# Kernel tuning notes

Measured on AMD Instinct MI355X. Metric: run time of the kernel, lower is better.

The kernel has to match this reference:

```python
import jax, jax.numpy as jnp
import numpy as np

BLANK = 1   # Offsets.GO
NEG = -1e30  # effective -inf that stays finite under logaddexp


def setup_inputs() -> dict:
    key = jax.random.key(0)
    k1, k2, k3, k4 = jax.random.split(key, 4)
    T, B, V, S = 1000, 64, 512, 100
    logits = jax.random.normal(k1, (T, B, V), dtype=jnp.float32)
    log_prob = jax.nn.log_softmax(logits, axis=-1)  # ctc_loss expects log-probs
    input_lengths = jax.random.randint(k2, (B,), T // 2, T + 1, dtype=jnp.int32)
    # target tokens avoid PAD(0)/GO(1,blank)/EOS(2), matching the masked_select semantics
    targets = jax.random.randint(k3, (B, S), 3, V, dtype=jnp.int32)
    target_lengths = jax.random.randint(k4, (B,), S // 2, S + 1, dtype=jnp.int32)
    return {"log_prob": log_prob, "input_lengths": input_lengths,
            "targets": targets, "target_lengths": target_lengths}


def _ctc_loss_sum(log_prob, input_lengths, targets, target_lengths):
    # log_prob: (T, B, V) log-softmax outputs; targets: (B, S) padded labels
    T, B, V = log_prob.shape
    S = targets.shape[1]
    Se = 2 * S + 1  # extended label sequence: blank-interleaved

    ext = jnp.full((B, Se), BLANK, dtype=targets.dtype).at[:, 1::2].set(targets)
    pos = jnp.arange(Se)
    ext_len = 2 * target_lengths + 1                      # (B,)
    valid = pos[None, :] < ext_len[:, None]               # (B, Se)
    ext_m2 = jnp.pad(ext[:, :-2], ((0, 0), (2, 0)), constant_values=BLANK)
    allow_skip = (ext != BLANK) & (ext != ext_m2) & (pos[None, :] >= 2)

    # emit[t, b, s] = log_prob[t, b, ext[b, s]]  -> (T, B, Se)
    emit = jnp.take_along_axis(log_prob, jnp.broadcast_to(ext[None], (T, B, Se)), axis=2)

    # alpha init at t=0
    alpha = jnp.full((B, Se), NEG, dtype=log_prob.dtype)
    alpha = alpha.at[:, 0].set(emit[0, :, 0])
    alpha = alpha.at[:, 1].set(jnp.where(target_lengths > 0, emit[0, :, 1], NEG))
    alpha = jnp.where(valid, alpha, NEG)

    def step(alpha, xt):
        emit_t, t = xt
        a1 = alpha
        a2 = jnp.pad(alpha[:, :-1], ((0, 0), (1, 0)), constant_values=NEG)
        a3 = jnp.where(allow_skip,
                       jnp.pad(alpha[:, :-2], ((0, 0), (2, 0)), constant_values=NEG),
                       NEG)
        new = jnp.logaddexp(jnp.logaddexp(a1, a2), a3) + emit_t
        new = jnp.where(valid, new, NEG)
        # freeze alpha once past each sample's input length
        alpha = jnp.where((t < input_lengths)[:, None], new, alpha)
        return alpha, None

    alpha, _ = jax.lax.scan(step, alpha, (emit[1:], jnp.arange(1, T)))

    last = 2 * target_lengths  # index of trailing blank in extended sequence
    a_last = jnp.take_along_axis(alpha, last[:, None], axis=1)[:, 0]
    a_prev = jnp.take_along_axis(alpha, jnp.maximum(last - 1, 0)[:, None], axis=1)[:, 0]
    loglik = jnp.logaddexp(a_last, a_prev)
    loss = -loglik
    # zero_infinity=True: infeasible alignments contribute 0
    loss = jnp.where(loglik < 0.5 * NEG, 0.0, loss)
    return jnp.sum(loss)  # reduction='sum'


def reference(log_prob, input_lengths, targets, target_lengths):
    return _ctc_loss_sum(log_prob, input_lengths, targets, target_lengths)
```

## Files before the change

### kernel.cpp

```cpp
#include <hip/hip_runtime.h>


#define NEGF (-1e30f)

constexpr int CT_T  = 1000;
constexpr int CT_B  = 64;
constexpr int CT_V  = 512;
constexpr int CT_S  = 100;
constexpr int CT_Se = 201;
constexpr float LOG2E = 1.4426950408889634f;
constexpr float LN2   = 0.6931471805599453f;
constexpr float SHIFT = 5.0f;

#if __has_builtin(__builtin_amdgcn_exp2f) && __has_builtin(__builtin_amdgcn_logf)
__device__ __forceinline__ float fexp2(float x) { return __builtin_amdgcn_exp2f(x); }
__device__ __forceinline__ float flog2(float x) { return __builtin_amdgcn_logf(x); }
__device__ __forceinline__ float frcp(float x)  { return __builtin_amdgcn_rcpf(x); }
#else
__device__ __forceinline__ float fexp2(float x) { return exp2f(x); }
__device__ __forceinline__ float flog2(float x) { return log2f(x); }
__device__ __forceinline__ float frcp(float x)  { return 1.0f / x; }
#endif

__device__ __forceinline__ float lae2_b2(float x, float y) {
    float m = fmaxf(x, y);
    float d = fminf(x, y) - m;
    return m + flog2(1.0f + fexp2(d));
}
__device__ __forceinline__ float lae3_b2(float x, float y, float z) {
    float m = fmaxf(fmaxf(x, y), z);
    float s = fexp2(x - m) + fexp2(y - m) + fexp2(z - m);
    return m + flog2(s);
}

__device__ __forceinline__ float wave_shr1(float x) {
    return __int_as_float(__builtin_amdgcn_update_dpp(
        0, __float_as_int(x), 0x138, 0xf, 0xf, true));
}
__device__ __forceinline__ float wave_max_nonneg(float x) {
#define DPPMAX(ctrl) x = fmaxf(x, __int_as_float(__builtin_amdgcn_update_dpp( \
        0, __float_as_int(x), ctrl, 0xf, 0xf, true)))
    DPPMAX(0x111); DPPMAX(0x112); DPPMAX(0x114); DPPMAX(0x118);
    DPPMAX(0x142); DPPMAX(0x143);
#undef DPPMAX
    return __int_as_float(__builtin_amdgcn_readlane(__float_as_int(x), 63));
}

typedef const __attribute__((address_space(1))) unsigned int* as1_uint_ptr;
typedef __attribute__((address_space(3))) unsigned int* as3_uint_ptr;
__device__ __forceinline__ void gld16(const void* g, void* l) {
    __builtin_amdgcn_global_load_lds((as1_uint_ptr)g, (as3_uint_ptr)l, 16, 0, 0);
}
__device__ __forceinline__ void waitcnt_vm32() { __builtin_amdgcn_s_waitcnt(0x8F70); }
__device__ __forceinline__ void waitcnt_vm0()  { __builtin_amdgcn_s_waitcnt(0x0F70); }

__global__ __launch_bounds__(64, 1) void ctc_alpha(
    const float* __restrict__ logp,
    const int*   __restrict__ in_len,
    const int*   __restrict__ tgt,
    const int*   __restrict__ tgt_len,
    float*       __restrict__ loss_ws)
{
    __shared__ float ldsr[4][8][CT_V];

    const int b    = blockIdx.x;
    const int lane = threadIdx.x;
    const int Tin  = in_len[b];
    const int Lt   = tgt_len[b];
    const int lim  = 2 * Lt + 1;
    const int* tg  = tgt + b * CT_S;

    const int s0 = 4 * lane, s1 = s0 + 1, s3 = s0 + 3;
    const int i1 = min((s1 - 1) >> 1, CT_S - 1);
    const int i3 = min((s3 - 1) >> 1, CT_S - 1);
    const int c1 = tg[i1];
    const int c3 = tg[i3];
    const float sk1 = ((s1 >= 3) && (s1 < CT_Se) && (c1 != tg[max(i1 - 1, 0)])) ? 1.f : 0.f;
    const float sk3 = ((s3 >= 3) && (s3 < CT_Se) && (c3 != tg[max(i3 - 1, 0)])) ? 1.f : 0.f;
    const float m0 = (s0     < lim) ? 1.f : 0.f;
    const float m1 = (s0 + 1 < lim) ? 1.f : 0.f;
    const float m2 = (s0 + 2 < lim) ? 1.f : 0.f;
    const float m3 = (s0 + 3 < lim) ? 1.f : 0.f;

    float a0 = 0.f, a1 = 0.f, a2 = 0.f, a3 = 0.f, pa3 = 0.f;
    if (lane == 0) {
        const float* r0 = logp + (size_t)b * CT_V;
        a0 = fexp2(fmaf(r0[1], LOG2E, SHIFT));
        if (Lt > 0) a1 = fexp2(fmaf(r0[c1], LOG2E, SHIFT));
    }
    float rs = 0.f;

    auto issue = [&](int k, int buf) {
        const int tb = 1 + 8 * k;
        #pragma unroll
        for (int i = 0; i < 8; ++i) {
            const int t = min(tb + i, CT_T - 1);
            const char* g = (const char*)(logp + ((size_t)t * CT_B + b) * CT_V)
                          + (size_t)lane * 16;
            gld16(g,        &ldsr[buf][i][0]);
            gld16(g + 1024, &ldsr[buf][i][256]);
        }
    };

    auto renorm = [&]() {
        float lm = wave_max_nonneg(fmaxf(fmaxf(a0, a1), fmaxf(a2, a3)));
        if (lm > 0.f) {
            float sc = frcp(lm);
            rs += flog2(lm);
            a0 *= sc; a1 *= sc; a2 *= sc; a3 *= sc;
            pa3 = wave_shr1(a3);
        }
    };

    auto run8 = [&](int buf, int tb, bool guard) {
        unsigned base = (unsigned)(size_t)(&ldsr[buf][0][0]);
        unsigned ab = base + 4u * 1;
        unsigned a1a = base + 4u * (unsigned)c1;
        unsigned a3a = base + 4u * (unsigned)c3;
        float g0,g1,g2,g3,g4,g5,g6,g7,g8,g9,g10,g11,
              g12,g13,g14,g15,g16,g17,g18,g19,g20,g21,g22,g23;
        asm volatile(
            "ds_read_b32 %0,  %24 offset:0\n\t"
            "ds_read_b32 %1,  %25 offset:0\n\t"
            "ds_read_b32 %2,  %26 offset:0\n\t"
            "ds_read_b32 %3,  %24 offset:2048\n\t"
            "ds_read_b32 %4,  %25 offset:2048\n\t"
            "ds_read_b32 %5,  %26 offset:2048\n\t"
            "ds_read_b32 %6,  %24 offset:4096\n\t"
            "ds_read_b32 %7,  %25 offset:4096\n\t"
            "ds_read_b32 %8,  %26 offset:4096\n\t"
            "ds_read_b32 %9,  %24 offset:6144\n\t"
            "ds_read_b32 %10, %25 offset:6144\n\t"
            "ds_read_b32 %11, %26 offset:6144\n\t"
            "ds_read_b32 %12, %24 offset:8192\n\t"
            "ds_read_b32 %13, %25 offset:8192\n\t"
            "ds_read_b32 %14, %26 offset:8192\n\t"
            "ds_read_b32 %15, %24 offset:10240\n\t"
            "ds_read_b32 %16, %25 offset:10240\n\t"
            "ds_read_b32 %17, %26 offset:10240\n\t"
            "ds_read_b32 %18, %24 offset:12288\n\t"
            "ds_read_b32 %19, %25 offset:12288\n\t"
            "ds_read_b32 %20, %26 offset:12288\n\t"
            "ds_read_b32 %21, %24 offset:14336\n\t"
            "ds_read_b32 %22, %25 offset:14336\n\t"
            "ds_read_b32 %23, %26 offset:14336\n\t"
            "s_waitcnt lgkmcnt(0)"
            : "=&v"(g0), "=&v"(g1), "=&v"(g2), "=&v"(g3), "=&v"(g4), "=&v"(g5),
              "=&v"(g6), "=&v"(g7), "=&v"(g8), "=&v"(g9), "=&v"(g10), "=&v"(g11),
              "=&v"(g12), "=&v"(g13), "=&v"(g14), "=&v"(g15), "=&v"(g16), "=&v"(g17),
              "=&v"(g18), "=&v"(g19), "=&v"(g20), "=&v"(g21), "=&v"(g22), "=&v"(g23)
            : "v"(ab), "v"(a1a), "v"(a3a));

        float eb[8], e1[8], e3[8];
        float gb[24] = {g0,g1,g2,g3,g4,g5,g6,g7,g8,g9,g10,g11,
                        g12,g13,g14,g15,g16,g17,g18,g19,g20,g21,g22,g23};
        #pragma unroll
        for (int i = 0; i < 8; ++i) {
            eb[i] = fexp2(fmaf(gb[3 * i],     LOG2E, SHIFT));
            e1[i] = fexp2(fmaf(gb[3 * i + 1], LOG2E, SHIFT));
            e3[i] = fexp2(fmaf(gb[3 * i + 2], LOG2E, SHIFT));
        }
        #pragma unroll
        for (int i = 0; i < 8; ++i) {
            float ex = eb[i] * m0, ey = e1[i] * m1;
            float ez = eb[i] * m2, ew = e3[i] * m3;
            float n0 = (a0 + pa3) * ex;
            float n1 = fmaf(sk1, pa3, a1 + a0) * ey;
            float n2 = (a2 + a1) * ez;
            float n3 = fmaf(sk3, a1, a3 + a2) * ew;
            if (!guard || (tb + i < Tin)) { a0 = n0; a1 = n1; a2 = n2; a3 = n3; }
            pa3 = wave_shr1(a3);
        }
    };

    issue(0, 0); issue(1, 1); issue(2, 2);
    const int Kf = (Tin - 1) / 8;
    const int K  = (Tin - 1 + 7) / 8;
    for (int k = 0; k < Kf; ++k) {
        waitcnt_vm32();
        issue(k + 3, (k + 3) & 3);
        run8(k & 3, 0, false);
        if (k & 1) renorm();
    }
    if (K > Kf) {
        waitcnt_vm32();
        run8(Kf & 3, 1 + 8 * Kf, true);
    }
    waitcnt_vm0();

    const int last = 2 * Lt;
    const int prev = max(last - 1, 0);
    const int lr = last & 3, lidx = last >> 2;
    float av = (lr == 0) ? a0 : (lr == 1) ? a1 : (lr == 2) ? a2 : a3;
    float a_last = __shfl(av, lidx);
    const int pr = prev & 3, pidx = prev >> 2;
    float pv = (pr == 0) ? a0 : (pr == 1) ? a1 : (pr == 2) ? a2 : a3;
    float a_prev = __shfl(pv, pidx);

    float sum = a_last + a_prev;
    float loss = 0.f;
    if (sum > 0.f)
        loss = -(flog2(sum) + rs - SHIFT * (float)Tin) * LN2;
    if (lane == 0) loss_ws[b] = loss;
}

__global__ __launch_bounds__(64) void ctc_alpha_fb(
    const float* __restrict__ logp, const int* __restrict__ in_len,
    const int* __restrict__ tgt, const int* __restrict__ tgt_len,
    float* __restrict__ loss_ws)
{
    const int b = blockIdx.x, lane = threadIdx.x;
    const int Tin = in_len[b], Lt = tgt_len[b];
    const int ext_len = 2 * Lt + 1;
    const int* tg = tgt + b * CT_S;
    const int s0 = 4 * lane, s1 = s0 + 1, s3 = s0 + 3;
    const int i1 = min((s1 - 1) >> 1, CT_S - 1);
    const int i3 = min((s3 - 1) >> 1, CT_S - 1);
    const int c1 = tg[i1], c3 = tg[i3];
    const bool skip1 = (s1 >= 3) && (s1 < CT_Se) && (c1 != tg[max(i1 - 1, 0)]);
    const bool skip3 = (s3 >= 3) && (s3 < CT_Se) && (c3 != tg[max(i3 - 1, 0)]);
    const bool v0 = s0 < ext_len, v1 = s1 < ext_len;
    const bool v2 = (s0 + 2) < ext_len, v3 = s3 < ext_len;
    const float* row0 = logp + (long long)b * CT_V;
    const long long stride = (long long)CT_B * CT_V;
    float a0 = NEGF, a1 = NEGF, a2 = NEGF, a3 = NEGF;
    if (lane == 0) {
        a0 = row0[1] * LOG2E;
        if (ext_len > 1) a1 = row0[c1] * LOG2E;
    }
    float3 E0, E1, E2, E3;
    auto ld = [&](float3& e, int t) {
        int tt = min(t, CT_T - 1);
        const float* r = row0 + (long long)tt * stride;
        e.x = r[1] * LOG2E; e.y = r[c1] * LOG2E; e.z = r[c3] * LOG2E;
    };
    auto step = [&](const float3& e) {
        float pa3 = __shfl_up(a3, 1);
        if (lane == 0) pa3 = NEGF;
        float z1 = skip1 ? pa3 : NEGF;
        float z3 = skip3 ? a1 : NEGF;
        float n0 = v0 ? lae2_b2(a0, pa3)    + e.x : NEGF;
        float n1 = v1 ? lae3_b2(a1, a0, z1) + e.y : NEGF;
        float n2 = v2 ? lae2_b2(a2, a1)     + e.x : NEGF;
        float n3 = v3 ? lae3_b2(a3, a2, z3) + e.z : NEGF;
        a0 = n0; a1 = n1; a2 = n2; a3 = n3;
    };
    ld(E0, 1); ld(E1, 2); ld(E2, 3); ld(E3, 4);
    for (int t = 1; t < Tin; t += 4) {
        step(E0); ld(E0, t + 4);
        if (t + 1 < Tin) { step(E1); ld(E1, t + 5); }
        if (t + 2 < Tin) { step(E2); ld(E2, t + 6); }
        if (t + 3 < Tin) { step(E3); ld(E3, t + 7); }
    }
    const int last = 2 * Lt, prev = max(last - 1, 0);
    const int lr = last & 3, lidx = last >> 2;
    float av = (lr == 0) ? a0 : (lr == 1) ? a1 : (lr == 2) ? a2 : a3;
    float a_last = __shfl(av, lidx);
    const int pr = prev & 3, pidx = prev >> 2;
    float pv = (pr == 0) ? a0 : (pr == 1) ? a1 : (pr == 2) ? a2 : a3;
    float a_prev = __shfl(pv, pidx);
    float loglik = lae2_b2(a_last, a_prev) * LN2;
    float loss = (loglik < 0.5f * NEGF) ? 0.0f : -loglik;
    if (lane == 0) loss_ws[b] = loss;
}

__global__ __launch_bounds__(64) void ctc_sum(const float* __restrict__ loss_ws,
                                              float* __restrict__ out)
{
    float v = loss_ws[threadIdx.x];
    #pragma unroll
    for (int o = 32; o > 0; o >>= 1) v += __shfl_down(v, o);
    if (threadIdx.x == 0) out[0] = v;
}

extern "C" void kernel_launch(void* const* d_in, const int* in_sizes, int n_in,
                              void* d_out, int out_size, void* d_ws, size_t ws_size,
                              hipStream_t stream) {
    const float* logp    = (const float*)d_in[0];
    const int*   in_len  = (const int*)d_in[1];
    const int*   tgt     = (const int*)d_in[2];
    const int*   tgt_len = (const int*)d_in[3];
    float* out = (float*)d_out;
    float* loss_ws = (float*)d_ws;

    if (ws_size >= 256 * sizeof(float)) {
        hipLaunchKernelGGL(ctc_alpha, dim3(CT_B), dim3(64), 0, stream,
                           logp, in_len, tgt, tgt_len, loss_ws);
    } else {
        hipLaunchKernelGGL(ctc_alpha_fb, dim3(CT_B), dim3(64), 0, stream,
                           logp, in_len, tgt, tgt_len, loss_ws);
    }
    hipLaunchKernelGGL(ctc_sum, dim3(1), dim3(64), 0, stream, loss_ws, out);
}
```

Before: 228.4 us.

## Split CTC alpha into compute wave and three loader waves with barrier pipeline

Launches 256 threads per block: wave 0 runs the alpha recursion while waves 1-3 take turns issuing the global-to-LDS prefetch of 8-step logprob chunks, with a block barrier each chunk. The aim is to take the load issue and vmcnt waits off the serial compute wave's critical path. In exchange it adds a block-wide s_barrier per 8 timesteps. Correctness relies on loader waves waiting on their own vmcnt before the barrier that precedes consumption; an error in that ordering could let wave 0 read LDS data that has not arrived.

```diff
diff --git a/kernel.cpp b/kernel.cpp
--- a/kernel.cpp
+++ b/kernel.cpp
@@ -51,10 +51,8 @@
 __device__ __forceinline__ void gld16(const void* g, void* l) {
     __builtin_amdgcn_global_load_lds((as1_uint_ptr)g, (as3_uint_ptr)l, 16, 0, 0);
 }
-__device__ __forceinline__ void waitcnt_vm32() { __builtin_amdgcn_s_waitcnt(0x8F70); }
-__device__ __forceinline__ void waitcnt_vm0()  { __builtin_amdgcn_s_waitcnt(0x0F70); }
-
-__global__ __launch_bounds__(64, 1) void ctc_alpha(
+
+__global__ __launch_bounds__(256, 1) void ctc_alpha(
     const float* __restrict__ logp,
     const int*   __restrict__ in_len,
     const int*   __restrict__ tgt,
@@ -64,11 +62,16 @@
     __shared__ float ldsr[4][8][CT_V];
 
     const int b    = blockIdx.x;
-    const int lane = threadIdx.x;
+    const int tid  = threadIdx.x;
+    const int wv   = tid >> 6;
+    const int lane = tid & 63;
     const int Tin  = in_len[b];
     const int Lt   = tgt_len[b];
     const int lim  = 2 * Lt + 1;
     const int* tg  = tgt + b * CT_S;
+
+    const int Kf = (Tin - 1) / 8;
+    const int K  = (Tin - 1 + 7) / 8;
 
     const int s0 = 4 * lane, s1 = s0 + 1, s3 = s0 + 3;
     const int i1 = min((s1 - 1) >> 1, CT_S - 1);
@@ -83,7 +86,7 @@
     const float m3 = (s0 + 3 < lim) ? 1.f : 0.f;
 
     float a0 = 0.f, a1 = 0.f, a2 = 0.f, a3 = 0.f, pa3 = 0.f;
-    if (lane == 0) {
+    if (tid == 0) {
         const float* r0 = logp + (size_t)b * CT_V;
         a0 = fexp2(fmaf(r0[1], LOG2E, SHIFT));
         if (Lt > 0) a1 = fexp2(fmaf(r0[c1], LOG2E, SHIFT));
@@ -173,20 +176,31 @@
         }
     };
 
-    issue(0, 0); issue(1, 1); issue(2, 2);
-    const int Kf = (Tin - 1) / 8;
-    const int K  = (Tin - 1 + 7) / 8;
-    for (int k = 0; k < Kf; ++k) {
-        waitcnt_vm32();
-        issue(k + 3, (k + 3) & 3);
-        run8(k & 3, 0, false);
-        if (k & 1) renorm();
-    }
-    if (K > Kf) {
-        waitcnt_vm32();
-        run8(Kf & 3, 1 + 8 * Kf, true);
-    }
-    waitcnt_vm0();
+    if (wv) {
+        const int p = wv - 1;
+        if (p < K) issue(p, p);
+        if (p == 0)
+            asm volatile("s_waitcnt vmcnt(0)" ::: "memory");
+    }
+    __builtin_amdgcn_s_barrier();
+
+    for (int j = 0; j < K; ++j) {
+        if (wv == 0) {
+            if (j < Kf) { run8(j & 3, 0, false); if (j & 1) renorm(); }
+            else        run8(j & 3, 1 + 8 * j, true);
+        } else {
+            const int p = wv - 1;
+            if ((j % 3) == p && (j + 3) < K) issue(j + 3, (j + 3) & 3);
+            if (((j + 1) % 3) == p && (j + 1) < K)
+                asm volatile("s_waitcnt vmcnt(0)" ::: "memory");
+        }
+        __builtin_amdgcn_s_barrier();
+    }
+
+    if (wv) {
+        asm volatile("s_waitcnt vmcnt(0)" ::: "memory");
+        return;
+    }
 
     const int last = 2 * Lt;
     const int prev = max(last - 1, 0);
@@ -284,7 +298,7 @@
     float* loss_ws = (float*)d_ws;
 
     if (ws_size >= 256 * sizeof(float)) {
-        hipLaunchKernelGGL(ctc_alpha, dim3(CT_B), dim3(64), 0, stream,
+        hipLaunchKernelGGL(ctc_alpha, dim3(CT_B), dim3(256), 0, stream,
                            logp, in_len, tgt, tgt_len, loss_ws);
     } else {
         hipLaunchKernelGGL(ctc_alpha_fb, dim3(CT_B), dim3(64), 0, stream,
```

Measured after the change: 206.1 us. -9.7%, faster.

## Replace LDS-staged row prefetch with direct register gathers, triple-buffered

Applied to the files above, without the earlier changes.

Drops the global_load_lds staging of full 2KB logit rows into shared memory and the follow-up ds_read gathers. Each lane now loads only the three logits it needs (blank, c1, c3) straight into registers, with a three-deep rotation of register buffers and a 6-chunk unrolled loop. This cuts fetched bytes and LDS traffic, but issues scattered 4-byte global loads and leaves waits to compiler-inserted vmcnt, which may expose more latency on the serial recurrence.

```diff
diff --git a/kernel.cpp b/kernel.cpp
--- a/kernel.cpp
+++ b/kernel.cpp
@@ -46,14 +46,6 @@
     return __int_as_float(__builtin_amdgcn_readlane(__float_as_int(x), 63));
 }
 
-typedef const __attribute__((address_space(1))) unsigned int* as1_uint_ptr;
-typedef __attribute__((address_space(3))) unsigned int* as3_uint_ptr;
-__device__ __forceinline__ void gld16(const void* g, void* l) {
-    __builtin_amdgcn_global_load_lds((as1_uint_ptr)g, (as3_uint_ptr)l, 16, 0, 0);
-}
-__device__ __forceinline__ void waitcnt_vm32() { __builtin_amdgcn_s_waitcnt(0x8F70); }
-__device__ __forceinline__ void waitcnt_vm0()  { __builtin_amdgcn_s_waitcnt(0x0F70); }
-
 __global__ __launch_bounds__(64, 1) void ctc_alpha(
     const float* __restrict__ logp,
     const int*   __restrict__ in_len,
@@ -61,14 +53,14 @@
     const int*   __restrict__ tgt_len,
     float*       __restrict__ loss_ws)
 {
-    __shared__ float ldsr[4][8][CT_V];
-
     const int b    = blockIdx.x;
     const int lane = threadIdx.x;
     const int Tin  = in_len[b];
     const int Lt   = tgt_len[b];
     const int lim  = 2 * Lt + 1;
     const int* tg  = tgt + b * CT_S;
+
+    const int K = (Tin - 1 + 7) / 8;
 
     const int s0 = 4 * lane, s1 = s0 + 1, s3 = s0 + 3;
     const int i1 = min((s1 - 1) >> 1, CT_S - 1);
@@ -90,15 +82,19 @@
     }
     float rs = 0.f;
 
-    auto issue = [&](int k, int buf) {
+    float gb0[8], g10[8], g30[8];
+    float gb1[8], g11[8], g31[8];
+    float gb2[8], g12[8], g32[8];
+
+    auto iss = [&](float (&gb)[8], float (&g1a)[8], float (&g3a)[8], int k) {
         const int tb = 1 + 8 * k;
         #pragma unroll
         for (int i = 0; i < 8; ++i) {
             const int t = min(tb + i, CT_T - 1);
-            const char* g = (const char*)(logp + ((size_t)t * CT_B + b) * CT_V)
-                          + (size_t)lane * 16;
-            gld16(g,        &ldsr[buf][i][0]);
-            gld16(g + 1024, &ldsr[buf][i][256]);
+            const float* r = logp + ((size_t)t * CT_B + b) * CT_V;
+            gb[i]  = r[1];
+            g1a[i] = r[c1];
+            g3a[i] = r[c3];
         }
     };
 
@@ -112,53 +108,14 @@
         }
     };
 
-    auto run8 = [&](int buf, int tb, bool guard) {
-        unsigned base = (unsigned)(size_t)(&ldsr[buf][0][0]);
-        unsigned ab = base + 4u * 1;
-        unsigned a1a = base + 4u * (unsigned)c1;
-        unsigned a3a = base + 4u * (unsigned)c3;
-        float g0,g1,g2,g3,g4,g5,g6,g7,g8,g9,g10,g11,
-              g12,g13,g14,g15,g16,g17,g18,g19,g20,g21,g22,g23;
-        asm volatile(
-            "ds_read_b32 %0,  %24 offset:0\n\t"
-            "ds_read_b32 %1,  %25 offset:0\n\t"
-            "ds_read_b32 %2,  %26 offset:0\n\t"
-            "ds_read_b32 %3,  %24 offset:2048\n\t"
-            "ds_read_b32 %4,  %25 offset:2048\n\t"
-            "ds_read_b32 %5,  %26 offset:2048\n\t"
-            "ds_read_b32 %6,  %24 offset:4096\n\t"
-            "ds_read_b32 %7,  %25 offset:4096\n\t"
-            "ds_read_b32 %8,  %26 offset:4096\n\t"
-            "ds_read_b32 %9,  %24 offset:6144\n\t"
-            "ds_read_b32 %10, %25 offset:6144\n\t"
-            "ds_read_b32 %11, %26 offset:6144\n\t"
-            "ds_read_b32 %12, %24 offset:8192\n\t"
-            "ds_read_b32 %13, %25 offset:8192\n\t"
-            "ds_read_b32 %14, %26 offset:8192\n\t"
-            "ds_read_b32 %15, %24 offset:10240\n\t"
-            "ds_read_b32 %16, %25 offset:10240\n\t"
-            "ds_read_b32 %17, %26 offset:10240\n\t"
-            "ds_read_b32 %18, %24 offset:12288\n\t"
-            "ds_read_b32 %19, %25 offset:12288\n\t"
-            "ds_read_b32 %20, %26 offset:12288\n\t"
-            "ds_read_b32 %21, %24 offset:14336\n\t"
-            "ds_read_b32 %22, %25 offset:14336\n\t"
-            "ds_read_b32 %23, %26 offset:14336\n\t"
-            "s_waitcnt lgkmcnt(0)"
-            : "=&v"(g0), "=&v"(g1), "=&v"(g2), "=&v"(g3), "=&v"(g4), "=&v"(g5),
-              "=&v"(g6), "=&v"(g7), "=&v"(g8), "=&v"(g9), "=&v"(g10), "=&v"(g11),
-              "=&v"(g12), "=&v"(g13), "=&v"(g14), "=&v"(g15), "=&v"(g16), "=&v"(g17),
-              "=&v"(g18), "=&v"(g19), "=&v"(g20), "=&v"(g21), "=&v"(g22), "=&v"(g23)
-            : "v"(ab), "v"(a1a), "v"(a3a));
-
+    auto proc = [&](float (&gb)[8], float (&g1a)[8], float (&g3a)[8],
+                    int tb, bool guard) {
         float eb[8], e1[8], e3[8];
-        float gb[24] = {g0,g1,g2,g3,g4,g5,g6,g7,g8,g9,g10,g11,
-                        g12,g13,g14,g15,g16,g17,g18,g19,g20,g21,g22,g23};
         #pragma unroll
         for (int i = 0; i < 8; ++i) {
-            eb[i] = fexp2(fmaf(gb[3 * i],     LOG2E, SHIFT));
-            e1[i] = fexp2(fmaf(gb[3 * i + 1], LOG2E, SHIFT));
-            e3[i] = fexp2(fmaf(gb[3 * i + 2], LOG2E, SHIFT));
+            eb[i] = fexp2(fmaf(gb[i],  LOG2E, SHIFT));
+            e1[i] = fexp2(fmaf(g1a[i], LOG2E, SHIFT));
+            e3[i] = fexp2(fmaf(g3a[i], LOG2E, SHIFT));
         }
         #pragma unroll
         for (int i = 0; i < 8; ++i) {
@@ -173,20 +130,33 @@
         }
     };
 
-    issue(0, 0); issue(1, 1); issue(2, 2);
-    const int Kf = (Tin - 1) / 8;
-    const int K  = (Tin - 1 + 7) / 8;
-    for (int k = 0; k < Kf; ++k) {
-        waitcnt_vm32();
-        issue(k + 3, (k + 3) & 3);
-        run8(k & 3, 0, false);
-        if (k & 1) renorm();
-    }
-    if (K > Kf) {
-        waitcnt_vm32();
-        run8(Kf & 3, 1 + 8 * Kf, true);
-    }
-    waitcnt_vm0();
+    iss(gb0, g10, g30, 0);
+    iss(gb1, g11, g31, 1);
+    iss(gb2, g12, g32, 2);
+
+    int j = 0;
+    for (; j + 6 < K; j += 6) {
+        proc(gb0, g10, g30, 1 + 8 * j,       false);           iss(gb0, g10, g30, j + 3);
+        proc(gb1, g11, g31, 1 + 8 * (j + 1), false); renorm(); iss(gb1, g11, g31, j + 4);
+        proc(gb2, g12, g32, 1 + 8 * (j + 2), false);           iss(gb2, g12, g32, j + 5);
+        proc(gb0, g10, g30, 1 + 8 * (j + 3), false); renorm(); iss(gb0, g10, g30, j + 6);
+        proc(gb1, g11, g31, 1 + 8 * (j + 4), false);           iss(gb1, g11, g31, j + 7);
+        proc(gb2, g12, g32, 1 + 8 * (j + 5), false); renorm(); iss(gb2, g12, g32, j + 8);
+    }
+    for (; j < K; ++j) {
+        const int s = j % 3;
+        if (s == 0) {
+            proc(gb0, g10, g30, 1 + 8 * j, true);
+            if (j + 3 < K) iss(gb0, g10, g30, j + 3);
+        } else if (s == 1) {
+            proc(gb1, g11, g31, 1 + 8 * j, true);
+            if (j + 3 < K) iss(gb1, g11, g31, j + 3);
+        } else {
+            proc(gb2, g12, g32, 1 + 8 * j, true);
+            if (j + 3 < K) iss(gb2, g12, g32, j + 3);
+        }
+        if (j & 1) renorm();
+    }
 
     const int last = 2 * Lt;
     const int prev = max(last - 1, 0);
```

After: 236.7 us. 3.7% more time.
